# Kernel optimization log

Hardware: AMD Instinct MI355X
Metric: run time of the kernel (lower is better)

The kernel has to match this reference:

```python
import jax, jax.numpy as jnp
import numpy as np

B, T, D, H = 32, 2048, 512, 512


def setup_inputs() -> dict:
    key = jax.random.key(0)
    k1, k2 = jax.random.split(key)
    x = jax.random.normal(k1, (B, T, D), dtype=jnp.float32)
    # Linear(D+H -> 4H); xavier-uniform-ish init
    limit = float(np.sqrt(6.0 / ((D + H) + 4 * H)))
    W = jax.random.uniform(k2, (D + H, 4 * H), minval=-limit, maxval=limit, dtype=jnp.float32)
    b = jnp.zeros((4 * H,), dtype=jnp.float32)
    b = b.at[H:2 * H].set(1.0)  # forget-gate bias init = 1
    h0 = jnp.zeros((B, H), dtype=jnp.float32)
    c0 = jnp.zeros((B, H), dtype=jnp.float32)
    return {"x": x, "W": W, "b": b, "h0": h0, "c0": c0}


def reference(x, W, b, h0, c0):
    # Split weight into input and hidden parts to avoid per-step concat.
    Wx, Wh = W[:D], W[D:]  # (D,4H), (H,4H)
    # Precompute input projections for all timesteps: (T,B,4H)
    xg = jnp.einsum('btd,dg->tbg', x, Wx) + b

    def step(carry, xg_t):
        h, c = carry
        gates = xg_t + h @ Wh  # (B,4H)
        i, f, g, o = jnp.split(gates, 4, axis=-1)
        i = jax.nn.sigmoid(i)
        f = jax.nn.sigmoid(f)
        g = jnp.tanh(g)
        o = jax.nn.sigmoid(o)
        c_t = f * c + i * g
        h_t = o * jnp.tanh(c_t)
        return (h_t, c_t), h_t

    (h_T, c_T), hs = jax.lax.scan(step, (h0, c0), xg)  # hs: (T,B,H)
    outputs = jnp.transpose(hs, (1, 0, 2))  # (B,T,H)
    return outputs, (h_T, c_T)
```

## Files before the change

kernel.cpp:

```cpp
#include <hip/hip_runtime.h>

#define TT 2048
#define BB 32
#define DD 512
#define HH 512
#define NWG 64
#define NTHR 256

typedef short s8v __attribute__((ext_vector_type(8)));
typedef float f4v __attribute__((ext_vector_type(4)));
typedef unsigned u4v __attribute__((ext_vector_type(4)));

union UF { u4v u; s8v s; };

__device__ __forceinline__ float asf(unsigned u) { return __uint_as_float(u); }

__device__ __forceinline__ unsigned cvtpk(float a, float b) {
    unsigned r;
    asm("v_cvt_pk_bf16_f32 %0, %1, %2" : "=v"(r) : "v"(a), "v"(b));
    return r;
}
__device__ __forceinline__ void split2(float a, float b, unsigned& hp, unsigned& lp) {
    hp = cvtpk(a, b);
    lp = cvtpk(a - asf(hp << 16), b - asf(hp & 0xFFFF0000u));
}

__global__ void lstm_init(const float* __restrict__ h0, const float* __restrict__ c0,
                          unsigned* __restrict__ hhi, unsigned* __restrict__ hlo,
                          float* __restrict__ cbuf, unsigned* __restrict__ flags) {
    int j = blockIdx.x * blockDim.x + threadIdx.x;
    if (j < NWG * 16) flags[j] = 0u;
    if (j < BB * HH / 2) {
        unsigned hp, lp;
        split2(h0[2 * j], h0[2 * j + 1], hp, lp);
        hhi[j] = hp;
        hlo[j] = lp;
    }
    cbuf[j] = c0[j];
}

__global__ __launch_bounds__(NTHR) void gemm_xg(
    const float* __restrict__ x, const float* __restrict__ W,
    const float* __restrict__ bias, float* __restrict__ xg, int t0)
{
    const int wg  = blockIdx.x & 63;
    const int tcb = blockIdx.x >> 6;
    const int tid = threadIdx.x;
    const int u0  = wg * 8;
    const int wv  = tid >> 6, ln = tid & 63;
    const int bh  = wv >> 1, ch = wv & 1;
    const int fl  = ln & 15, fg = ln >> 4;

    s8v whi[16], wlo[16];
    const int col  = ch * 16 + fl;
    const int wcol = ((col >> 3) << 9) + u0 + (col & 7);
    #pragma unroll
    for (int it = 0; it < 16; ++it) {
        float v[8];
        #pragma unroll
        for (int j = 0; j < 8; ++j)
            v[j] = W[(size_t)(it * 32 + fg * 8 + j) * 2048 + wcol];
        UF H, L;
        #pragma unroll
        for (int q = 0; q < 4; ++q) {
            unsigned hp, lp;
            split2(v[2 * q], v[2 * q + 1], hp, lp);
            H.u[q] = hp; L.u[q] = lp;
        }
        whi[it] = H.s; wlo[it] = L.s;
    }
    const float bcol = bias[wcol];

    const int arow = bh * 16 + fl;
    const float* xlane = x + (size_t)arow * TT * DD + fg * 8;

    for (int ii = 0; ii < 64; ++ii) {
        const int i = tcb * 64 + ii;
        const int t = t0 + i;
        f4v acc  = {0.f, 0.f, 0.f, 0.f};
        f4v accl = {0.f, 0.f, 0.f, 0.f};
        const float* xs = xlane + (size_t)t * DD;
        #pragma unroll
        for (int it = 0; it < 16; ++it) {
            float4 f0 = *(const float4*)(xs + it * 32);
            float4 f1 = *(const float4*)(xs + it * 32 + 4);
            UF H, L;
            unsigned hp, lp;
            split2(f0.x, f0.y, hp, lp); H.u[0] = hp; L.u[0] = lp;
            split2(f0.z, f0.w, hp, lp); H.u[1] = hp; L.u[1] = lp;
            split2(f1.x, f1.y, hp, lp); H.u[2] = hp; L.u[2] = lp;
            split2(f1.z, f1.w, hp, lp); H.u[3] = hp; L.u[3] = lp;
            acc  = __builtin_amdgcn_mfma_f32_16x16x32_bf16(H.s, whi[it], acc, 0, 0, 0);
            accl = __builtin_amdgcn_mfma_f32_16x16x32_bf16(L.s, whi[it], accl, 0, 0, 0);
            accl = __builtin_amdgcn_mfma_f32_16x16x32_bf16(H.s, wlo[it], accl, 0, 0, 0);
        }
        float* dst = xg + ((size_t)i * NWG + wg) * 1024;
        #pragma unroll
        for (int r = 0; r < 4; ++r)
            dst[(bh * 16 + fg * 4 + r) * 32 + ch * 16 + fl] = acc[r] + accl[r] + bcol;
    }
}

__global__ __launch_bounds__(NTHR, 1) void lstm_scan(
    const float* __restrict__ W,
    const float* __restrict__ xg,
    float* __restrict__ out,
    unsigned* hhi, unsigned* hlo,
    float* __restrict__ cbuf,
    unsigned* flags, int t0, int nt)
{
    __shared__ float P[32][33];

    const int wg  = blockIdx.x;
    const int tid = threadIdx.x;
    const int u0  = wg * 8;
    const int wv  = tid >> 6, ln = tid & 63;
    const int bh  = wv >> 1, ch = wv & 1;
    const int fl  = ln & 15, fg = ln >> 4;

    s8v whi[16], wlo[16];
    {
        const int col  = ch * 16 + fl;
        const int wcol = ((col >> 3) << 9) + u0 + (col & 7);
        #pragma unroll
        for (int it = 0; it < 16; ++it) {
            float v[8];
            #pragma unroll
            for (int j = 0; j < 8; ++j)
                v[j] = W[(size_t)(512 + it * 32 + fg * 8 + j) * 2048 + wcol];
            UF H, L;
            #pragma unroll
            for (int q = 0; q < 4; ++q) {
                unsigned hp, lp;
                split2(v[2 * q], v[2 * q + 1], hp, lp);
                H.u[q] = hp; L.u[q] = lp;
            }
            whi[it] = H.s; wlo[it] = L.s;
        }
    }

    const int em = tid >> 3, ei = tid & 7;
    float cst = cbuf[em * HH + u0 + ei];

    const int arow = bh * 16 + fl;
    const int hb   = arow * (HH / 2) + fg * 4;
    const int crow = bh * 16 + fg * 4;
    const int ccol = ch * 16 + fl;

    for (int i = 0; i < nt; ++i) {
        const int t = t0 + i;

        float xgv[4];
        {
            const float* src = xg + ((size_t)i * NWG + wg) * 1024 + crow * 32 + ccol;
            #pragma unroll
            for (int r = 0; r < 4; ++r) xgv[r] = src[r * 32];
        }

        if (t > 0) {
            if (tid < 64) {
                for (;;) {
                    unsigned v = __hip_atomic_load(&flags[tid * 16], __ATOMIC_RELAXED,
                                                   __HIP_MEMORY_SCOPE_AGENT);
                    if (__all((int)v >= t)) break;
                }
            }
            __syncthreads();
            __builtin_amdgcn_fence(__ATOMIC_ACQUIRE, "agent");
        }

        f4v acc  = {0.f, 0.f, 0.f, 0.f};
        f4v accl = {0.f, 0.f, 0.f, 0.f};
        {
            const unsigned* hh = hhi + (size_t)(t & 1) * (BB * HH / 2);
            const unsigned* hl = hlo + (size_t)(t & 1) * (BB * HH / 2);
            #pragma unroll
            for (int it = 0; it < 16; ++it) {
                UF H, L;
                H.u = *(const u4v*)(hh + hb + it * 16);
                L.u = *(const u4v*)(hl + hb + it * 16);
                acc  = __builtin_amdgcn_mfma_f32_16x16x32_bf16(H.s, whi[it], acc, 0, 0, 0);
                accl = __builtin_amdgcn_mfma_f32_16x16x32_bf16(L.s, whi[it], accl, 0, 0, 0);
                accl = __builtin_amdgcn_mfma_f32_16x16x32_bf16(H.s, wlo[it], accl, 0, 0, 0);
            }
        }

        #pragma unroll
        for (int r = 0; r < 4; ++r)
            P[crow + r][ccol] = acc[r] + accl[r] + xgv[r];
        __syncthreads();

        float gi = P[em][ei];
        float gf = P[em][8 + ei];
        float gg = P[em][16 + ei];
        float go = P[em][24 + ei];
        float si = 1.0f / (1.0f + __expf(-gi));
        float sf = 1.0f / (1.0f + __expf(-gf));
        float e2 = __expf(2.0f * fminf(fmaxf(gg, -15.f), 15.f));
        float tg = (e2 - 1.0f) / (e2 + 1.0f);
        float so = 1.0f / (1.0f + __expf(-go));
        cst = sf * cst + si * tg;
        float e2c = __expf(2.0f * fminf(fmaxf(cst, -15.f), 15.f));
        float h = so * (e2c - 1.0f) / (e2c + 1.0f);

        {
            float hn = __shfl_down(h, 1);
            if ((ei & 1) == 0) {
                unsigned hp, lp;
                split2(h, hn, hp, lp);
                int idx = em * (HH / 2) + ((u0 + ei) >> 1);
                unsigned* dh = hhi + (size_t)((t + 1) & 1) * (BB * HH / 2);
                unsigned* dl = hlo + (size_t)((t + 1) & 1) * (BB * HH / 2);
                __hip_atomic_store(&dh[idx], hp, __ATOMIC_RELAXED, __HIP_MEMORY_SCOPE_AGENT);
                __hip_atomic_store(&dl[idx], lp, __ATOMIC_RELAXED, __HIP_MEMORY_SCOPE_AGENT);
            }
        }
        __syncthreads();
        if (tid == 0)
            __hip_atomic_store(&flags[wg * 16], (unsigned)(t + 1),
                               __ATOMIC_RELAXED, __HIP_MEMORY_SCOPE_AGENT);

        out[(size_t)em * TT * HH + (size_t)t * HH + u0 + ei] = h;
        if (t == TT - 1) {
            size_t ho = (size_t)BB * TT * HH;
            out[ho + em * HH + u0 + ei] = h;
            out[ho + (size_t)BB * HH + em * HH + u0 + ei] = cst;
        }
    }

    cbuf[em * HH + u0 + ei] = cst;
}

extern "C" void kernel_launch(void* const* d_in, const int* in_sizes, int n_in,
                              void* d_out, int out_size, void* d_ws, size_t ws_size,
                              hipStream_t stream) {
    const float* x  = nullptr;
    const float* W  = nullptr;
    const float* b  = nullptr;
    const float* h0 = nullptr;
    const float* c0 = nullptr;
    for (int i = 0; i < n_in; ++i) {
        int sz = in_sizes[i];
        if      (sz == BB * TT * DD)       x = (const float*)d_in[i];
        else if (sz == (DD + HH) * 4 * HH) W = (const float*)d_in[i];
        else if (sz == 4 * HH)             b = (const float*)d_in[i];
        else if (sz == BB * HH) { if (!h0) h0 = (const float*)d_in[i];
                                  else     c0 = (const float*)d_in[i]; }
    }
    float* out = (float*)d_out;

    char* base = (char*)d_ws;
    unsigned* hhi   = (unsigned*)(base);
    unsigned* hlo   = (unsigned*)(base + 65536);
    float*    cbuf  = (float*)   (base + 131072);
    unsigned* flags = (unsigned*)(base + 196608);
    float*    xg    = (float*)   (base + 200704);

    size_t avail = (ws_size > 200704) ? ws_size - 200704 : 0;
    size_t maxT  = avail / (NWG * BB * 32 * sizeof(float));
    int Tc = (int)((maxT / 64) * 64);
    if (Tc > TT) Tc = TT;
    if (Tc < 64) Tc = 64;

    lstm_init<<<64, NTHR, 0, stream>>>(h0, c0, hhi, hlo, cbuf, flags);

    for (int t0 = 0; t0 < TT; t0 += Tc) {
        int nt = (TT - t0 < Tc) ? (TT - t0) : Tc;
        gemm_xg<<<(nt / 64) * 64, NTHR, 0, stream>>>(x, W, b, xg, t0);
        lstm_scan<<<NWG, NTHR, 0, stream>>>(W, xg, out, hhi, hlo, cbuf, flags, t0, nt);
    }
}
```

Before: 16.18 ms.

## Shrink scan grid to 16 workgroups and drop bf16 split-precision for recurrence

The recurrent scan now runs on 16 workgroups of 1024 threads, each owning 32 hidden units, instead of 64 workgroups of 256. Fewer workgroups means fewer flags to poll at the per-step grid barrier. The hidden-state matmul drops the hi/lo bf16 split and runs a single bf16 MFMA per k-step, which removes the hlo buffer and two thirds of the MFMAs on the critical path. The xg layout changes to a plain (t, b, 4H) order and the bias-plus-input term is added after the shared-memory reduction. The cost is lower precision in h@Wh, since both h and Wh are now rounded to plain bf16, and more work per workgroup on each step.

```diff
diff --git a/kernel.cpp b/kernel.cpp
--- a/kernel.cpp
+++ b/kernel.cpp
@@ -4,7 +4,8 @@
 #define BB 32
 #define DD 512
 #define HH 512
-#define NWG 64
+#define NWGS 16
+#define STHR 1024
 #define NTHR 256
 
 typedef short s8v __attribute__((ext_vector_type(8)));
@@ -26,16 +27,11 @@
 }
 
 __global__ void lstm_init(const float* __restrict__ h0, const float* __restrict__ c0,
-                          unsigned* __restrict__ hhi, unsigned* __restrict__ hlo,
-                          float* __restrict__ cbuf, unsigned* __restrict__ flags) {
+                          unsigned* __restrict__ hhi, float* __restrict__ cbuf,
+                          unsigned* __restrict__ flags) {
     int j = blockIdx.x * blockDim.x + threadIdx.x;
-    if (j < NWG * 16) flags[j] = 0u;
-    if (j < BB * HH / 2) {
-        unsigned hp, lp;
-        split2(h0[2 * j], h0[2 * j + 1], hp, lp);
-        hhi[j] = hp;
-        hlo[j] = lp;
-    }
+    if (j < NWGS * 16) flags[j] = 0u;
+    if (j < BB * HH / 2) hhi[j] = cvtpk(h0[2 * j], h0[2 * j + 1]);
     cbuf[j] = c0[j];
 }
 
@@ -43,23 +39,23 @@
     const float* __restrict__ x, const float* __restrict__ W,
     const float* __restrict__ bias, float* __restrict__ xg, int t0)
 {
-    const int wg  = blockIdx.x & 63;
+    const int wg8 = blockIdx.x & 63;
     const int tcb = blockIdx.x >> 6;
     const int tid = threadIdx.x;
-    const int u0  = wg * 8;
+    const int u0  = wg8 * 8;
     const int wv  = tid >> 6, ln = tid & 63;
     const int bh  = wv >> 1, ch = wv & 1;
     const int fl  = ln & 15, fg = ln >> 4;
 
     s8v whi[16], wlo[16];
-    const int col  = ch * 16 + fl;
-    const int wcol = ((col >> 3) << 9) + u0 + (col & 7);
+    const int col32 = ch * 16 + fl;
+    const int gcol  = ((col32 >> 3) << 9) + u0 + (col32 & 7);
     #pragma unroll
     for (int it = 0; it < 16; ++it) {
         float v[8];
         #pragma unroll
         for (int j = 0; j < 8; ++j)
-            v[j] = W[(size_t)(it * 32 + fg * 8 + j) * 2048 + wcol];
+            v[j] = W[(size_t)(it * 32 + fg * 8 + j) * 2048 + gcol];
         UF H, L;
         #pragma unroll
         for (int q = 0; q < 4; ++q) {
@@ -69,7 +65,7 @@
         }
         whi[it] = H.s; wlo[it] = L.s;
     }
-    const float bcol = bias[wcol];
+    const float bcol = bias[gcol];
 
     const int arow = bh * 16 + fl;
     const float* xlane = x + (size_t)arow * TT * DD + fg * 8;
@@ -94,74 +90,66 @@
             accl = __builtin_amdgcn_mfma_f32_16x16x32_bf16(L.s, whi[it], accl, 0, 0, 0);
             accl = __builtin_amdgcn_mfma_f32_16x16x32_bf16(H.s, wlo[it], accl, 0, 0, 0);
         }
-        float* dst = xg + ((size_t)i * NWG + wg) * 1024;
+        float* dst = xg + (size_t)i * (BB * 2048);
         #pragma unroll
         for (int r = 0; r < 4; ++r)
-            dst[(bh * 16 + fg * 4 + r) * 32 + ch * 16 + fl] = acc[r] + accl[r] + bcol;
-    }
-}
-
-__global__ __launch_bounds__(NTHR, 1) void lstm_scan(
+            dst[(size_t)(bh * 16 + fg * 4 + r) * 2048 + gcol] = acc[r] + accl[r] + bcol;
+    }
+}
+
+__global__ __launch_bounds__(STHR, 1) void lstm_scan(
     const float* __restrict__ W,
     const float* __restrict__ xg,
     float* __restrict__ out,
-    unsigned* hhi, unsigned* hlo,
+    unsigned* hhi,
     float* __restrict__ cbuf,
     unsigned* flags, int t0, int nt)
 {
-    __shared__ float P[32][33];
+    __shared__ float P[32][132];
 
     const int wg  = blockIdx.x;
     const int tid = threadIdx.x;
-    const int u0  = wg * 8;
+    const int u0  = wg * 32;
     const int wv  = tid >> 6, ln = tid & 63;
-    const int bh  = wv >> 1, ch = wv & 1;
+    const int bh  = wv & 1;
+    const int cq  = wv >> 1;
     const int fl  = ln & 15, fg = ln >> 4;
 
-    s8v whi[16], wlo[16];
+    s8v whi[16];
     {
-        const int col  = ch * 16 + fl;
-        const int wcol = ((col >> 3) << 9) + u0 + (col & 7);
+        const int wcol = (cq >> 1) * 512 + u0 + (cq & 1) * 16 + fl;
         #pragma unroll
         for (int it = 0; it < 16; ++it) {
-            float v[8];
-            #pragma unroll
-            for (int j = 0; j < 8; ++j)
-                v[j] = W[(size_t)(512 + it * 32 + fg * 8 + j) * 2048 + wcol];
-            UF H, L;
+            UF H;
             #pragma unroll
             for (int q = 0; q < 4; ++q) {
-                unsigned hp, lp;
-                split2(v[2 * q], v[2 * q + 1], hp, lp);
-                H.u[q] = hp; L.u[q] = lp;
-            }
-            whi[it] = H.s; wlo[it] = L.s;
-        }
-    }
-
-    const int em = tid >> 3, ei = tid & 7;
+                float a = W[(size_t)(512 + it * 32 + fg * 8 + 2 * q) * 2048 + wcol];
+                float b = W[(size_t)(512 + it * 32 + fg * 8 + 2 * q + 1) * 2048 + wcol];
+                H.u[q] = cvtpk(a, b);
+            }
+            whi[it] = H.s;
+        }
+    }
+
+    const int em = tid >> 5, ei = tid & 31;
     float cst = cbuf[em * HH + u0 + ei];
 
     const int arow = bh * 16 + fl;
-    const int hb   = arow * (HH / 2) + fg * 4;
-    const int crow = bh * 16 + fg * 4;
-    const int ccol = ch * 16 + fl;
+    const int hb   = arow * 256;
 
     for (int i = 0; i < nt; ++i) {
         const int t = t0 + i;
 
-        float xgv[4];
-        {
-            const float* src = xg + ((size_t)i * NWG + wg) * 1024 + crow * 32 + ccol;
-            #pragma unroll
-            for (int r = 0; r < 4; ++r) xgv[r] = src[r * 32];
-        }
+        const float* xs = xg + (size_t)i * (BB * 2048) + em * 2048 + u0 + ei;
+        float xgi = xs[0], xgf = xs[512], xgg = xs[1024], xgo = xs[1536];
 
         if (t > 0) {
             if (tid < 64) {
                 for (;;) {
-                    unsigned v = __hip_atomic_load(&flags[tid * 16], __ATOMIC_RELAXED,
-                                                   __HIP_MEMORY_SCOPE_AGENT);
+                    unsigned v = (tid < NWGS)
+                        ? __hip_atomic_load(&flags[tid * 16], __ATOMIC_RELAXED,
+                                            __HIP_MEMORY_SCOPE_AGENT)
+                        : (unsigned)t;
                     if (__all((int)v >= t)) break;
                 }
             }
@@ -169,31 +157,25 @@
             __builtin_amdgcn_fence(__ATOMIC_ACQUIRE, "agent");
         }
 
-        f4v acc  = {0.f, 0.f, 0.f, 0.f};
-        f4v accl = {0.f, 0.f, 0.f, 0.f};
+        f4v acc = {0.f, 0.f, 0.f, 0.f};
         {
             const unsigned* hh = hhi + (size_t)(t & 1) * (BB * HH / 2);
-            const unsigned* hl = hlo + (size_t)(t & 1) * (BB * HH / 2);
             #pragma unroll
             for (int it = 0; it < 16; ++it) {
-                UF H, L;
-                H.u = *(const u4v*)(hh + hb + it * 16);
-                L.u = *(const u4v*)(hl + hb + it * 16);
-                acc  = __builtin_amdgcn_mfma_f32_16x16x32_bf16(H.s, whi[it], acc, 0, 0, 0);
-                accl = __builtin_amdgcn_mfma_f32_16x16x32_bf16(L.s, whi[it], accl, 0, 0, 0);
-                accl = __builtin_amdgcn_mfma_f32_16x16x32_bf16(H.s, wlo[it], accl, 0, 0, 0);
-            }
-        }
-
+                UF H;
+                H.u = *(const u4v*)(hh + hb + it * 16 + fg * 4);
+                acc = __builtin_amdgcn_mfma_f32_16x16x32_bf16(H.s, whi[it], acc, 0, 0, 0);
+            }
+        }
         #pragma unroll
         for (int r = 0; r < 4; ++r)
-            P[crow + r][ccol] = acc[r] + accl[r] + xgv[r];
+            P[bh * 16 + fg * 4 + r][cq * 16 + fl] = acc[r];
         __syncthreads();
 
-        float gi = P[em][ei];
-        float gf = P[em][8 + ei];
-        float gg = P[em][16 + ei];
-        float go = P[em][24 + ei];
+        float gi = xgi + P[em][ei];
+        float gf = xgf + P[em][32 + ei];
+        float gg = xgg + P[em][64 + ei];
+        float go = xgo + P[em][96 + ei];
         float si = 1.0f / (1.0f + __expf(-gi));
         float sf = 1.0f / (1.0f + __expf(-gf));
         float e2 = __expf(2.0f * fminf(fmaxf(gg, -15.f), 15.f));
@@ -206,13 +188,10 @@
         {
             float hn = __shfl_down(h, 1);
             if ((ei & 1) == 0) {
-                unsigned hp, lp;
-                split2(h, hn, hp, lp);
-                int idx = em * (HH / 2) + ((u0 + ei) >> 1);
+                unsigned hp = cvtpk(h, hn);
                 unsigned* dh = hhi + (size_t)((t + 1) & 1) * (BB * HH / 2);
-                unsigned* dl = hlo + (size_t)((t + 1) & 1) * (BB * HH / 2);
-                __hip_atomic_store(&dh[idx], hp, __ATOMIC_RELAXED, __HIP_MEMORY_SCOPE_AGENT);
-                __hip_atomic_store(&dl[idx], lp, __ATOMIC_RELAXED, __HIP_MEMORY_SCOPE_AGENT);
+                __hip_atomic_store(&dh[em * 256 + ((u0 + ei) >> 1)], hp,
+                                   __ATOMIC_RELAXED, __HIP_MEMORY_SCOPE_AGENT);
             }
         }
         __syncthreads();
@@ -251,22 +230,21 @@
 
     char* base = (char*)d_ws;
     unsigned* hhi   = (unsigned*)(base);
-    unsigned* hlo   = (unsigned*)(base + 65536);
-    float*    cbuf  = (float*)   (base + 131072);
-    unsigned* flags = (unsigned*)(base + 196608);
-    float*    xg    = (float*)   (base + 200704);
-
-    size_t avail = (ws_size > 200704) ? ws_size - 200704 : 0;
-    size_t maxT  = avail / (NWG * BB * 32 * sizeof(float));
+    float*    cbuf  = (float*)   (base + 65536);
+    unsigned* flags = (unsigned*)(base + 131072);
+    float*    xg    = (float*)   (base + 135168);
+
+    size_t avail = (ws_size > 135168) ? ws_size - 135168 : 0;
+    size_t maxT  = avail / (BB * 2048 * sizeof(float));
     int Tc = (int)((maxT / 64) * 64);
     if (Tc > TT) Tc = TT;
     if (Tc < 64) Tc = 64;
 
-    lstm_init<<<64, NTHR, 0, stream>>>(h0, c0, hhi, hlo, cbuf, flags);
+    lstm_init<<<64, NTHR, 0, stream>>>(h0, c0, hhi, cbuf, flags);
 
     for (int t0 = 0; t0 < TT; t0 += Tc) {
         int nt = (TT - t0 < Tc) ? (TT - t0) : Tc;
         gemm_xg<<<(nt / 64) * 64, NTHR, 0, stream>>>(x, W, b, xg, t0);
-        lstm_scan<<<NWG, NTHR, 0, stream>>>(W, xg, out, hhi, hlo, cbuf, flags, t0, nt);
-    }
-}
+        lstm_scan<<<NWGS, STHR, 0, stream>>>(W, xg, out, hhi, cbuf, flags, t0, nt);
+    }
+}
```

New measurement: 22.29 ms. 37.8% more time.
